# Performance work log

Measured on AMD Instinct MI355X. Metric: run time of the kernel, lower is better.

The kernel has to match this reference:

```python
import jax, jax.numpy as jnp
import numpy as np

B, S, E, H, NQ = 8, 2048, 8, 2, 8
D = E // H  # head_dim = 4
DIM = 2 ** NQ  # 256-amplitude state vector

# CNOT chain pattern from the module: (0,1),(1,2),...,(NQ-2,NQ-1),(NQ-1,0)
CNOTS = [(i, i + 1) for i in range(NQ - 1)] + [(NQ - 1, 0)]

# Pauli-Z sign table: wire 0 is the most-significant qubit axis (torchquantum convention)
_k = np.arange(DIM)
_SIGNS = (1.0 - 2.0 * ((_k[None, :] >> (NQ - 1 - np.arange(NQ))[:, None]) & 1)).astype(np.float32)  # (NQ, DIM)


def _quantum_measure(tok):
    """Batched simulation of the per-token circuit. tok: (N, E) real -> (N, NQ) <Z> values."""
    n = tok.shape[0]
    idx = jnp.arange(NQ) % D
    # encoder RX(tok[w]) then explicit RX(tok[w % head_dim]) on each wire: angles add.
    half = 0.5 * (tok[:, :NQ] + tok[:, idx])  # (N, NQ)
    a0 = jnp.cos(half).astype(jnp.complex64)
    a1 = (-1j) * jnp.sin(half).astype(jnp.complex64)
    qub = jnp.stack([a0, a1], axis=-1)  # (N, NQ, 2) per-qubit states (product state before CNOTs)
    # Kronecker product across the fixed NQ wires
    state = qub[:, 0, :]
    for w in range(1, NQ):
        state = (state[:, :, None] * qub[:, w, None, :]).reshape(n, -1)
    state = state.reshape((n,) + (2,) * NQ)
    # CNOT chain: flip target axis within control=1 block
    for c, t in CNOTS:
        c0 = jax.lax.index_in_dim(state, 0, c + 1, keepdims=True)
        c1 = jnp.flip(jax.lax.index_in_dim(state, 1, c + 1, keepdims=True), axis=t + 1)
        state = jnp.concatenate([c0, c1], axis=c + 1)
    p = (state.real ** 2 + state.imag ** 2).reshape(n, DIM)  # probabilities
    return p @ jnp.asarray(_SIGNS.T)  # (N, NQ) Pauli-Z expectations


def setup_inputs() -> dict:
    key = jax.random.key(0)
    ks = jax.random.split(key, 5)
    sc = 1.0 / np.sqrt(E)
    return {
        "x": jax.random.normal(ks[0], (B, S, E), jnp.float32),
        "Wq": jax.random.normal(ks[1], (E, E), jnp.float32) * sc,
        "Wk": jax.random.normal(ks[2], (E, E), jnp.float32) * sc,
        "Wv": jax.random.normal(ks[3], (E, E), jnp.float32) * sc,
        "Wo": jax.random.normal(ks[4], (E, E), jnp.float32) * sc,
    }


def reference(x, Wq, Wk, Wv, Wo):
    b, s, _ = x.shape
    # nn.Linear(bias=False): y = x @ W^T
    q = jnp.einsum('bse,fe->bsf', x, Wq).reshape(b, s, H, D)
    k = jnp.einsum('bse,fe->bsf', x, Wk).reshape(b, s, H, D)
    v = jnp.einsum('bse,fe->bsf', x, Wv).reshape(b, s, H, D)
    scores = jnp.einsum('bihd,bjhd->bhij', q, k) / jnp.sqrt(jnp.float32(D))
    attn = jax.nn.softmax(scores, axis=-1)  # dropout is identity at inference
    out = jnp.einsum('bhij,bjhd->bihd', attn, v).reshape(b, s, E)
    z = _quantum_measure(out.reshape(-1, E)).reshape(b, s, NQ)  # NQ == E
    return jnp.einsum('bsq,fq->bsf', z, Wo)
```

## Files before the change

### kernel.cpp

```cpp
#include <hip/hip_runtime.h>


#define SS 2048
#define EE 8

extern "C" __global__ __launch_bounds__(256)
void qa_attn3(const float* __restrict__ x, const float* __restrict__ Wq,
              const float* __restrict__ Wk, const float* __restrict__ Wv,
              float* __restrict__ wsD, float4* __restrict__ wsA) {
    __shared__ float wrow[96];
    __shared__ __align__(16) float4 kv4[512];
    __shared__ __align__(16) float4 racc[4 * 512];
    __shared__ float rden[4 * 512];

    const int bid = blockIdx.x;
    const int jw = bid & 7, rt = (bid >> 3) & 3, h = (bid >> 5) & 1, b = bid >> 6;
    const int tid = threadIdx.x, lane = tid & 63, w = tid >> 6;

    if (tid < 96) {
        const int grp = tid >> 5, d = (tid >> 3) & 3, e = tid & 7;
        const float* W = (grp == 0) ? Wq : (grp == 1 ? Wk : Wv);
        float val = W[(h * 4 + d) * EE + e];
        if (grp == 0) val *= 0.72134752044f;
        wrow[tid] = val;
    }
    __syncthreads();

    {
        const int j = jw * 256 + tid;
        const float* xp = x + ((size_t)(b * SS + j)) * EE;
        float xv[8];
        *(float4*)&xv[0] = *(const float4*)xp;
        *(float4*)&xv[4] = *(const float4*)(xp + 4);
        float kk[4], vv[4];
        #pragma unroll
        for (int d = 0; d < 4; ++d) {
            float sk = 0.f, sv = 0.f;
            #pragma unroll
            for (int e = 0; e < 8; ++e) {
                sk += xv[e] * wrow[32 + d * 8 + e];
                sv += xv[e] * wrow[64 + d * 8 + e];
            }
            kk[d] = sk; vv[d] = sv;
        }
        kv4[tid * 2]     = make_float4(kk[0], kk[1], kk[2], kk[3]);
        kv4[tid * 2 + 1] = make_float4(vv[0], vv[1], vv[2], vv[3]);
    }

    float q[8][4];
    const int row0 = rt * 512 + lane;
    #pragma unroll
    for (int m = 0; m < 8; ++m) {
        const float* xp = x + ((size_t)(b * SS + row0 + m * 64)) * EE;
        float xv[8];
        *(float4*)&xv[0] = *(const float4*)xp;
        *(float4*)&xv[4] = *(const float4*)(xp + 4);
        #pragma unroll
        for (int d = 0; d < 4; ++d) {
            float s = 0.f;
            #pragma unroll
            for (int e = 0; e < 8; ++e) s += xv[e] * wrow[d * 8 + e];
            q[m][d] = s;
        }
    }
    __syncthreads();

    float den[8] = {};
    float acc[8][4] = {};
    const int jb = w * 64;
    #pragma unroll 2
    for (int jl = 0; jl < 64; ++jl) {
        const float4 kk = kv4[(jb + jl) * 2];
        const float4 vv = kv4[(jb + jl) * 2 + 1];
        #pragma unroll
        for (int m = 0; m < 8; ++m) {
            const float s = q[m][0] * kk.x + q[m][1] * kk.y
                          + q[m][2] * kk.z + q[m][3] * kk.w;
            const float e = __builtin_amdgcn_exp2f(s);
            den[m] += e;
            acc[m][0] += e * vv.x; acc[m][1] += e * vv.y;
            acc[m][2] += e * vv.z; acc[m][3] += e * vv.w;
        }
    }

    #pragma unroll
    for (int m = 0; m < 8; ++m) {
        rden[w * 512 + lane + m * 64] = den[m];
        racc[w * 512 + lane + m * 64] =
            make_float4(acc[m][0], acc[m][1], acc[m][2], acc[m][3]);
    }
    __syncthreads();
    #pragma unroll
    for (int u = 0; u < 2; ++u) {
        const int r = tid + u * 256;
        float d = rden[r] + rden[512 + r] + rden[1024 + r] + rden[1536 + r];
        float4 a0 = racc[r], a1 = racc[512 + r], a2 = racc[1024 + r], a3 = racc[1536 + r];
        float4 a = make_float4(a0.x + a1.x + a2.x + a3.x,
                               a0.y + a1.y + a2.y + a3.y,
                               a0.z + a1.z + a2.z + a3.z,
                               a0.w + a1.w + a2.w + a3.w);
        const size_t idx = ((size_t)((b * 2 + h) * 8 + jw)) * SS + rt * 512 + r;
        wsD[idx] = d;
        wsA[idx] = a;
    }
}

extern "C" __global__ __launch_bounds__(256)
void qa_quantum3(const float* __restrict__ wsD, const float4* __restrict__ wsA,
                 const float* __restrict__ Wo, float* __restrict__ out) {
    __shared__ float wo[64];
    const int tid = threadIdx.x;
    if (tid < 64) wo[tid] = Wo[tid];
    __syncthreads();

    const int g = blockIdx.x * 256 + tid;
    const int b = g >> 11, s = g & 2047;

    float tok[8];
    #pragma unroll
    for (int h = 0; h < 2; ++h) {
        float den = 0.f, a0 = 0.f, a1 = 0.f, a2 = 0.f, a3 = 0.f;
        #pragma unroll
        for (int sl = 0; sl < 8; ++sl) {
            const size_t idx = ((size_t)((b * 2 + h) * 8 + sl)) * SS + s;
            den += wsD[idx];
            const float4 p = wsA[idx];
            a0 += p.x; a1 += p.y; a2 += p.z; a3 += p.w;
        }
        const float inv = 1.f / den;
        tok[h * 4 + 0] = a0 * inv; tok[h * 4 + 1] = a1 * inv;
        tok[h * 4 + 2] = a2 * inv; tok[h * 4 + 3] = a3 * inv;
    }

    float c[8];
    #pragma unroll
    for (int ww = 0; ww < 8; ++ww) c[ww] = __cosf(tok[ww] + tok[ww & 3]);

    float z[8];
    float p = 1.f;
    #pragma unroll
    for (int qq = 1; qq < 8; ++qq) { p *= c[qq]; z[qq] = p; }
    z[0] = p;
    #pragma unroll
    for (int qq = 1; qq < 8; ++qq) z[qq] *= c[0];

    float y[8];
    #pragma unroll
    for (int f = 0; f < 8; ++f) {
        float sum = 0.f;
        #pragma unroll
        for (int qq = 0; qq < 8; ++qq) sum += z[qq] * wo[f * 8 + qq];
        y[f] = sum;
    }
    float* op = out + (size_t)g * 8;
    *(float4*)op       = make_float4(y[0], y[1], y[2], y[3]);
    *(float4*)(op + 4) = make_float4(y[4], y[5], y[6], y[7]);
}

extern "C" void kernel_launch(void* const* d_in, const int* in_sizes, int n_in,
                              void* d_out, int out_size, void* d_ws, size_t ws_size,
                              hipStream_t stream) {
    const float* x  = (const float*)d_in[0];
    const float* Wq = (const float*)d_in[1];
    const float* Wk = (const float*)d_in[2];
    const float* Wv = (const float*)d_in[3];
    const float* Wo = (const float*)d_in[4];
    float* out = (float*)d_out;

    float*  wsD = (float*)d_ws;
    float4* wsA = (float4*)((char*)d_ws + (16 * 8 * 2048) * sizeof(float));

    qa_attn3<<<dim3(512), dim3(256), 0, stream>>>(x, Wq, Wk, Wv, wsD, wsA);
    qa_quantum3<<<dim3(64), dim3(256), 0, stream>>>(wsD, wsA, Wo, out);
}
```

Before: 87.24 us.

## Split key range across twice as many blocks and use polynomial exp2

Each attention block now covers 128 keys instead of 256, which doubles the grid to 1024 blocks, and the quantum kernel sums 16 partial results instead of 8. Wave 0 now does the reduction straight from its own registers, so the shared buffers shrink and occupancy can rise to 4 blocks per CU. The hardware exp2 is replaced with a cubic polynomial plus ldexp, moving the work onto the FMA units at the cost of some accuracy. The trade-off is more per-block setup (Q projection and weight loads) and twice the workspace traffic.

Result: slower. 98.27 us (+12.6%).

```diff
diff --git a/kernel.cpp b/kernel.cpp
--- a/kernel.cpp
+++ b/kernel.cpp
@@ -4,17 +4,26 @@
 #define SS 2048
 #define EE 8
 
-extern "C" __global__ __launch_bounds__(256)
-void qa_attn3(const float* __restrict__ x, const float* __restrict__ Wq,
+__device__ __forceinline__ float fast_exp2(float s) {
+    const float n = rintf(s);
+    const float f = s - n;
+    float p = fmaf(f, 0.05550411f, 0.24022651f);
+    p = fmaf(f, p, 0.69314718f);
+    p = fmaf(f, p, 1.0f);
+    return __builtin_amdgcn_ldexpf(p, (int)n);
+}
+
+extern "C" __global__ __launch_bounds__(256, 4)
+void qa_attn4(const float* __restrict__ x, const float* __restrict__ Wq,
               const float* __restrict__ Wk, const float* __restrict__ Wv,
               float* __restrict__ wsD, float4* __restrict__ wsA) {
     __shared__ float wrow[96];
-    __shared__ __align__(16) float4 kv4[512];
-    __shared__ __align__(16) float4 racc[4 * 512];
-    __shared__ float rden[4 * 512];
+    __shared__ __align__(16) float4 kv4[256];
+    __shared__ float rden[3 * 512];
+    __shared__ __align__(16) float4 racc[3 * 512];
 
     const int bid = blockIdx.x;
-    const int jw = bid & 7, rt = (bid >> 3) & 3, h = (bid >> 5) & 1, b = bid >> 6;
+    const int jw = bid & 15, rt = (bid >> 4) & 3, h = (bid >> 6) & 1, b = bid >> 7;
     const int tid = threadIdx.x, lane = tid & 63, w = tid >> 6;
 
     if (tid < 96) {
@@ -26,8 +35,8 @@
     }
     __syncthreads();
 
-    {
-        const int j = jw * 256 + tid;
+    if (tid < 128) {
+        const int j = jw * 128 + tid;
         const float* xp = x + ((size_t)(b * SS + j)) * EE;
         float xv[8];
         *(float4*)&xv[0] = *(const float4*)xp;
@@ -67,46 +76,50 @@
 
     float den[8] = {};
     float acc[8][4] = {};
-    const int jb = w * 64;
+    const int jb = w * 32;
     #pragma unroll 2
-    for (int jl = 0; jl < 64; ++jl) {
+    for (int jl = 0; jl < 32; ++jl) {
         const float4 kk = kv4[(jb + jl) * 2];
         const float4 vv = kv4[(jb + jl) * 2 + 1];
         #pragma unroll
         for (int m = 0; m < 8; ++m) {
             const float s = q[m][0] * kk.x + q[m][1] * kk.y
                           + q[m][2] * kk.z + q[m][3] * kk.w;
-            const float e = __builtin_amdgcn_exp2f(s);
+            const float e = fast_exp2(s);
             den[m] += e;
             acc[m][0] += e * vv.x; acc[m][1] += e * vv.y;
             acc[m][2] += e * vv.z; acc[m][3] += e * vv.w;
         }
     }
 
-    #pragma unroll
-    for (int m = 0; m < 8; ++m) {
-        rden[w * 512 + lane + m * 64] = den[m];
-        racc[w * 512 + lane + m * 64] =
-            make_float4(acc[m][0], acc[m][1], acc[m][2], acc[m][3]);
+    if (w > 0) {
+        #pragma unroll
+        for (int m = 0; m < 8; ++m) {
+            rden[(w - 1) * 512 + lane + m * 64] = den[m];
+            racc[(w - 1) * 512 + lane + m * 64] =
+                make_float4(acc[m][0], acc[m][1], acc[m][2], acc[m][3]);
+        }
     }
     __syncthreads();
-    #pragma unroll
-    for (int u = 0; u < 2; ++u) {
-        const int r = tid + u * 256;
-        float d = rden[r] + rden[512 + r] + rden[1024 + r] + rden[1536 + r];
-        float4 a0 = racc[r], a1 = racc[512 + r], a2 = racc[1024 + r], a3 = racc[1536 + r];
-        float4 a = make_float4(a0.x + a1.x + a2.x + a3.x,
-                               a0.y + a1.y + a2.y + a3.y,
-                               a0.z + a1.z + a2.z + a3.z,
-                               a0.w + a1.w + a2.w + a3.w);
-        const size_t idx = ((size_t)((b * 2 + h) * 8 + jw)) * SS + rt * 512 + r;
-        wsD[idx] = d;
-        wsA[idx] = a;
+    if (w == 0) {
+        #pragma unroll
+        for (int m = 0; m < 8; ++m) {
+            const int r = lane + m * 64;
+            float d = den[m] + rden[r] + rden[512 + r] + rden[1024 + r];
+            float4 a1 = racc[r], a2 = racc[512 + r], a3 = racc[1024 + r];
+            float4 a = make_float4(acc[m][0] + a1.x + a2.x + a3.x,
+                                   acc[m][1] + a1.y + a2.y + a3.y,
+                                   acc[m][2] + a1.z + a2.z + a3.z,
+                                   acc[m][3] + a1.w + a2.w + a3.w);
+            const size_t idx = ((size_t)((b * 2 + h) * 16 + jw)) * SS + row0 + m * 64;
+            wsD[idx] = d;
+            wsA[idx] = a;
+        }
     }
 }
 
 extern "C" __global__ __launch_bounds__(256)
-void qa_quantum3(const float* __restrict__ wsD, const float4* __restrict__ wsA,
+void qa_quantum4(const float* __restrict__ wsD, const float4* __restrict__ wsA,
                  const float* __restrict__ Wo, float* __restrict__ out) {
     __shared__ float wo[64];
     const int tid = threadIdx.x;
@@ -121,8 +134,8 @@
     for (int h = 0; h < 2; ++h) {
         float den = 0.f, a0 = 0.f, a1 = 0.f, a2 = 0.f, a3 = 0.f;
         #pragma unroll
-        for (int sl = 0; sl < 8; ++sl) {
-            const size_t idx = ((size_t)((b * 2 + h) * 8 + sl)) * SS + s;
+        for (int sl = 0; sl < 16; ++sl) {
+            const size_t idx = ((size_t)((b * 2 + h) * 16 + sl)) * SS + s;
             den += wsD[idx];
             const float4 p = wsA[idx];
             a0 += p.x; a1 += p.y; a2 += p.z; a3 += p.w;
@@ -168,8 +181,8 @@
     float* out = (float*)d_out;
 
     float*  wsD = (float*)d_ws;
-    float4* wsA = (float4*)((char*)d_ws + (16 * 8 * 2048) * sizeof(float));
+    float4* wsA = (float4*)((char*)d_ws + (16 * 16 * 2048) * sizeof(float));
 
-    qa_attn3<<<dim3(512), dim3(256), 0, stream>>>(x, Wq, Wk, Wv, wsD, wsA);
-    qa_quantum3<<<dim3(64), dim3(256), 0, stream>>>(wsD, wsA, Wo, out);
+    qa_attn4<<<dim3(1024), dim3(256), 0, stream>>>(x, Wq, Wk, Wv, wsD, wsA);
+    qa_quantum4<<<dim3(64), dim3(256), 0, stream>>>(wsD, wsA, Wo, out);
 }
```
